# Kernel tuning notes

Hardware: AMD Instinct MI355X
Metric: run time of the kernel (lower is better)

Reference implementation:

```python
import jax, jax.numpy as jnp
import numpy as np

H = 256            # hidden_size
S = 4              # num_of_steps
B = 512            # reactions
N_MOLS = B * S     # 2048 molecules
ATOMS_PER_MOL = 32
N_ATOMS = N_MOLS * ATOMS_PER_MOL   # 65536
BONDS_PER_MOL = 64
N_BONDS = N_MOLS * BONDS_PER_MOL   # 131072 directed bonds (+1 pad row)
MAX_NB = 6
ATOM_FDIM = 133
BOND_FDIM = 147
DEPTH = 3
N_ITERS = 3  # Set2Set iterations


def setup_inputs() -> dict:
    key = jax.random.key(0)
    ks = jax.random.split(key, 20)
    def p(k, shape):
        return jax.random.normal(k, shape, jnp.float32) * 0.02
    inp = {}
    inp['f_atoms'] = jax.random.normal(ks[0], (N_ATOMS, ATOM_FDIM), jnp.float32)
    f_bonds = jax.random.normal(ks[1], (N_BONDS + 1, BOND_FDIM), jnp.float32)
    inp['f_bonds'] = f_bonds.at[0].set(0.0)  # chemprop zero pad row
    inp['a2b'] = jax.random.randint(ks[2], (N_ATOMS, MAX_NB), 0, N_BONDS + 1)
    inp['b2a'] = jax.random.randint(ks[3], (N_BONDS + 1,), 0, N_ATOMS)
    inp['b2revb'] = jax.random.randint(ks[4], (N_BONDS + 1,), 0, N_BONDS + 1)
    # MPN weights (bias=False for W_i/W_h as in args.bias default)
    inp['W_i'] = p(ks[5], (BOND_FDIM, H))
    inp['W_h'] = p(ks[6], (H, H))
    inp['W_o'] = p(ks[7], (ATOM_FDIM + H, H)); inp['b_o'] = jnp.zeros((H,), jnp.float32)
    # NNAttention over steps
    inp['W_nn0'] = p(ks[8], (2 * H, H));  inp['b_nn0'] = jnp.zeros((H,), jnp.float32)
    inp['W_nn0s'] = p(ks[9], (H, H));     inp['b_nn0s'] = jnp.zeros((H,), jnp.float32)
    inp['W_nn1'] = p(ks[10], (S * H, H)); inp['b_nn1'] = jnp.zeros((H,), jnp.float32)
    # node Set2Set (LSTM: input 2H -> hidden H) + condenser
    inp['lstm_n_Wih'] = p(ks[11], (4 * H, 2 * H))
    inp['lstm_n_Whh'] = p(ks[12], (4 * H, H))
    inp['lstm_n_b'] = jnp.zeros((4 * H,), jnp.float32)
    inp['node_cond_W'] = p(ks[13], (2 * H, H)); inp['node_cond_b'] = jnp.zeros((H,), jnp.float32)
    # graph (step) Set2Set + condenser
    inp['lstm_g_Wih'] = p(ks[14], (4 * H, 2 * H))
    inp['lstm_g_Whh'] = p(ks[15], (4 * H, H))
    inp['lstm_g_b'] = jnp.zeros((4 * H,), jnp.float32)
    inp['graph_cond_W'] = p(ks[16], (2 * H, H)); inp['graph_cond_b'] = jnp.zeros((H,), jnp.float32)
    return inp


def set2set(feat, Wih, Whh, b):
    # feat: [M, N, D]; LSTM n_layers=1, PyTorch gate order i,f,g,o
    M, N, D = feat.shape
    h = jnp.zeros((M, D), feat.dtype)
    c = jnp.zeros((M, D), feat.dtype)
    q_star = jnp.zeros((M, 2 * D), feat.dtype)
    for _ in range(N_ITERS):
        gates = q_star @ Wih.T + h @ Whh.T + b
        i, f, g, o = jnp.split(gates, 4, axis=-1)
        c = jax.nn.sigmoid(f) * c + jax.nn.sigmoid(i) * jnp.tanh(g)
        h = jax.nn.sigmoid(o) * jnp.tanh(c)
        q = h
        alpha = jax.nn.softmax(jnp.einsum('md,mnd->mn', q, feat), axis=1)
        readout = jnp.einsum('mn,mnd->md', alpha, feat)
        q_star = jnp.concatenate([q, readout], axis=-1)
    return q_star


def nn_attention(h, W0, b0, W0s, b0s, W1, b1):
    # vectorized form of the Attention module's s1/s2 double loop
    Bm, Sm, D = h.shape
    h1 = jnp.broadcast_to(h[:, :, None, :], (Bm, Sm, Sm, D))
    h2 = jnp.broadcast_to(h[:, None, :, :], (Bm, Sm, Sm, D))
    pair = jnp.concatenate([h1, h2], -1) @ W0 + b0          # [B,S,S,D] NN0(cat(h_s1,h_s2))
    self_o = h @ W0s + b0s                                   # [B,S,D]   NN0_self(h_s1)
    diag = jnp.eye(Sm, dtype=bool)[None, :, :, None]
    out = jnp.where(diag, self_o[:, :, None, :], pair)       # diagonal uses NN0_self
    return out.reshape(Bm, Sm, Sm * D) @ W1 + b1             # NN1 over s2-concat


def reference(f_atoms, f_bonds, a2b, b2a, b2revb, W_i, W_h, W_o, b_o,
              W_nn0, b_nn0, W_nn0s, b_nn0s, W_nn1, b_nn1,
              lstm_n_Wih, lstm_n_Whh, lstm_n_b, node_cond_W, node_cond_b,
              lstm_g_Wih, lstm_g_Whh, lstm_g_b, graph_cond_W, graph_cond_b):
    # --- bond message passing (chemprop, atom_messages=False) ---
    inp = f_bonds @ W_i                       # [NB+1, H], row 0 = 0 (no bias)
    message = jax.nn.relu(inp)
    message = message.at[0].set(0.0)          # keep pad row zero
    for _ in range(DEPTH - 1):
        a_message = message[a2b].sum(axis=1)          # gather+sum: [NA, H]
        msg = a_message[b2a] - message[b2revb]        # [NB+1, H]
        message = jax.nn.relu(inp + msg @ W_h)
        message = message.at[0].set(0.0)
    nei = message[a2b].sum(axis=1)                    # [NA, H]
    atom_h = jax.nn.relu(jnp.concatenate([f_atoms, nei], -1) @ W_o + b_o)
    # --- node readout: Set2Set per molecule + condenser ---
    feat = atom_h.reshape(N_MOLS, ATOMS_PER_MOL, H)
    mol = set2set(feat, lstm_n_Wih, lstm_n_Whh, lstm_n_b) @ node_cond_W + node_cond_b
    # --- step attention (NNAttention over num_of_steps) ---
    steps = mol.reshape(B, S, H)
    steps = nn_attention(steps, W_nn0, b_nn0, W_nn0s, b_nn0s, W_nn1, b_nn1)
    # --- step readout: Set2Set over steps + condenser ---
    out = set2set(steps, lstm_g_Wih, lstm_g_Whh, lstm_g_b) @ graph_cond_W + graph_cond_b
    return out  # [B, H]
```

## Files before the change

kernel.cpp:

```cpp
#include <hip/hip_runtime.h>
#include <math.h>

#define H 256
#define S_STEPS 4
#define B_RXN 512
#define N_MOLS 2048
#define ATOMS_PER_MOL 32
#define N_ATOMS 65536
#define N_BONDS 131072
#define NBP1 131073
#define MAX_NB 6
#define ATOM_FDIM 133
#define BOND_FDIM 147
#define DEPTH 3
#define N_ITERS 3

typedef unsigned short bf16u;
typedef __attribute__((ext_vector_type(8))) short short8v;
typedef __attribute__((ext_vector_type(4))) float f32x4;

__device__ __forceinline__ float b2f(bf16u u) {
    union { unsigned int i; float f; } c; c.i = ((unsigned int)u) << 16; return c.f;
}
__device__ __forceinline__ bf16u f2b(float f) {
    union { float f; unsigned int i; } c; c.f = f;
    unsigned int i = c.i;
    return (bf16u)((i + 0x7FFFu + ((i >> 16) & 1u)) >> 16);
}
__device__ __forceinline__ unsigned int relu2bf(unsigned int w) {
    unsigned int lo = w & 0xFFFFu, hi = w >> 16;
    if (lo & 0x8000u) lo = 0u;
    if (hi & 0x8000u) hi = 0u;
    return lo | (hi << 16);
}

template<int MODE, bool RELUA>
__global__ __launch_bounds__(512) void dense_gemm_k(
    const bf16u* __restrict__ A1,
    const bf16u* __restrict__ A2,
    const bf16u* __restrict__ WT,
    const float* __restrict__ bias,
    bf16u* __restrict__ outb,
    int M)
{
    constexpr int KP = (MODE == 0) ? 160 : ((MODE == 1) ? 256 : 416);
    constexpr int NS = KP / 32;
    __shared__ bf16u As[128][40];
    __shared__ bf16u Bs[256][40];

    const int tid = threadIdx.x;
    const int lane = tid & 63, w = tid >> 6;
    const int wr = w >> 2, wc = w & 3;
    const int m0 = blockIdx.x * 128;
    const int ar = tid >> 2, q8 = (tid & 3) * 8;
    const int br = tid >> 1, bh = (tid & 1) * 16;
    const int arow = m0 + ar;
    const bool rok = arow < M;
    const int lr = lane & 15, lk = (lane >> 4) * 8;
    const uint4 z4 = {0u, 0u, 0u, 0u};

    auto loadA = [&](int s) -> uint4 {
        const int kc = s * 32 + q8;
        if (MODE == 2) {
            return (kc < 160) ? *(const uint4*)(A1 + (size_t)arow * 160 + kc)
                              : *(const uint4*)(A2 + (size_t)arow * 256 + (kc - 160));
        } else {
            constexpr int LDA = (MODE == 0) ? 160 : 256;
            return rok ? *(const uint4*)(A1 + (size_t)arow * LDA + kc) : z4;
        }
    };
    auto loadB0 = [&](int s) { return *(const uint4*)(WT + (size_t)br * KP + s * 32 + bh); };
    auto loadB1 = [&](int s) { return *(const uint4*)(WT + (size_t)br * KP + s * 32 + bh + 8); };
    auto writeAB = [&](uint4 va, uint4 vb0, uint4 vb1) {
        if (RELUA) {
            va.x = relu2bf(va.x); va.y = relu2bf(va.y);
            va.z = relu2bf(va.z); va.w = relu2bf(va.w);
        }
        *(uint4*)&As[ar][q8] = va;
        *(uint4*)&Bs[br][bh] = vb0;
        *(uint4*)&Bs[br][bh + 8] = vb1;
    };

    f32x4 acc[4][4];
    const f32x4 zf = {0.f, 0.f, 0.f, 0.f};
    #pragma unroll
    for (int i = 0; i < 4; ++i)
        #pragma unroll
        for (int j = 0; j < 4; ++j) acc[i][j] = zf;

    writeAB(loadA(0), loadB0(0), loadB1(0));
    __syncthreads();

    for (int s = 0; s < NS; ++s) {
        const bool pf = (s + 1 < NS);
        uint4 va = z4, vb0 = z4, vb1 = z4;
        if (pf) { va = loadA(s + 1); vb0 = loadB0(s + 1); vb1 = loadB1(s + 1); }

        short8v a[4], b[4];
        #pragma unroll
        for (int mf = 0; mf < 4; ++mf)
            a[mf] = *(const short8v*)&As[wr * 64 + mf * 16 + lr][lk];
        #pragma unroll
        for (int nf = 0; nf < 4; ++nf)
            b[nf] = *(const short8v*)&Bs[wc * 64 + nf * 16 + lr][lk];
        #pragma unroll
        for (int mf = 0; mf < 4; ++mf)
            #pragma unroll
            for (int nf = 0; nf < 4; ++nf)
                acc[mf][nf] = __builtin_amdgcn_mfma_f32_16x16x32_bf16(
                    a[mf], b[nf], acc[mf][nf], 0, 0, 0);
        __syncthreads();
        if (pf) {
            writeAB(va, vb0, vb1);
            __syncthreads();
        }
    }

    const int rbase = (lane >> 4) * 4;
    #pragma unroll
    for (int mf = 0; mf < 4; ++mf) {
        #pragma unroll
        for (int nf = 0; nf < 4; ++nf) {
            const int col = wc * 64 + nf * 16 + lr;
            #pragma unroll
            for (int r = 0; r < 4; ++r) {
                const int row = m0 + wr * 64 + mf * 16 + rbase + r;
                if (row >= M) continue;
                float v = acc[mf][nf][r];
                const size_t off = (size_t)row * H + col;
                if (MODE == 2) {
                    v += bias[col];
                    outb[off] = f2b(fmaxf(v, 0.f));
                } else {
                    outb[off] = f2b(v);
                }
            }
        }
    }
}

__global__ __launch_bounds__(256) void combine_k(
    const bf16u* __restrict__ inp, const bf16u* __restrict__ AP,
    const bf16u* __restrict__ MW,
    const int* __restrict__ b2a, const int* __restrict__ b2revb,
    bf16u* __restrict__ msg)
{
    int idx = blockIdx.x * 256 + threadIdx.x;
    if (idx >= NBP1 * 32) return;
    int b = idx >> 5, c = (idx & 31) * 8;
    bf16u* op = msg + (size_t)b * H + c;
    if (b == 0) {
        *(uint4*)op = make_uint4(0u, 0u, 0u, 0u);
        return;
    }
    int a = b2a[b], rb = b2revb[b];
    uint4 ui = *(const uint4*)(inp + (size_t)b * H + c);
    uint4 up = *(const uint4*)(AP + (size_t)a * H + c);
    uint4 um = *(const uint4*)(MW + (size_t)rb * H + c);
    uint4 o;
    unsigned int* pi = &ui.x; unsigned int* pp = &up.x;
    unsigned int* pm = &um.x; unsigned int* po = &o.x;
    #pragma unroll
    for (int t = 0; t < 4; ++t) {
        float lo = b2f((bf16u)(pi[t] & 0xFFFFu)) + b2f((bf16u)(pp[t] & 0xFFFFu))
                 - b2f((bf16u)(pm[t] & 0xFFFFu));
        float hi = b2f((bf16u)(pi[t] >> 16)) + b2f((bf16u)(pp[t] >> 16))
                 - b2f((bf16u)(pm[t] >> 16));
        lo = fmaxf(lo, 0.f); hi = fmaxf(hi, 0.f);
        po[t] = (unsigned int)f2b(lo) | ((unsigned int)f2b(hi) << 16);
    }
    *(uint4*)op = o;
}

template<bool BIAS>
__global__ __launch_bounds__(256) void lin64_k(
    const float* __restrict__ A1, int lda1, int KA1,
    const float* __restrict__ A2, int lda2,
    const bf16u* __restrict__ WT, int ldw,
    const float* __restrict__ bias,
    float* __restrict__ C, int ldc, int K)
{
    __shared__ bf16u As[64][40];
    __shared__ bf16u Bs[64][40];
    const int tid = threadIdx.x;
    const int lane = tid & 63, w = tid >> 6;
    const int m0 = blockIdx.x * 64;
    const int col0 = blockIdx.y * 64;
    const int ar = tid >> 2, kq8 = (tid & 3) * 8;
    const int lr = lane & 15, lk = (lane >> 4) * 8;

    f32x4 acc[4];
    const f32x4 zf = {0.f, 0.f, 0.f, 0.f};
    #pragma unroll
    for (int j = 0; j < 4; ++j) acc[j] = zf;

    for (int k0 = 0; k0 < K; k0 += 32) {
        const float* src = (k0 < KA1)
            ? (A1 + (size_t)(m0 + ar) * lda1 + k0 + kq8)
            : (A2 + (size_t)(m0 + ar) * lda2 + (k0 - KA1) + kq8);
        float4 f0 = *(const float4*)src;
        float4 f1 = *(const float4*)(src + 4);
        ushort4 s0, s1;
        s0.x = f2b(f0.x); s0.y = f2b(f0.y); s0.z = f2b(f0.z); s0.w = f2b(f0.w);
        s1.x = f2b(f1.x); s1.y = f2b(f1.y); s1.z = f2b(f1.z); s1.w = f2b(f1.w);
        *(ushort4*)&As[ar][kq8] = s0;
        *(ushort4*)&As[ar][kq8 + 4] = s1;
        *(uint4*)&Bs[ar][kq8] = *(const uint4*)(WT + (size_t)(col0 + ar) * ldw + k0 + kq8);
        __syncthreads();

        short8v a = *(const short8v*)&As[w * 16 + lr][lk];
        short8v b[4];
        #pragma unroll
        for (int nf = 0; nf < 4; ++nf)
            b[nf] = *(const short8v*)&Bs[nf * 16 + lr][lk];
        #pragma unroll
        for (int nf = 0; nf < 4; ++nf)
            acc[nf] = __builtin_amdgcn_mfma_f32_16x16x32_bf16(a, b[nf], acc[nf], 0, 0, 0);
        __syncthreads();
    }

    const int rbase = (lane >> 4) * 4;
    #pragma unroll
    for (int nf = 0; nf < 4; ++nf) {
        const int col = col0 + nf * 16 + lr;
        #pragma unroll
        for (int r = 0; r < 4; ++r) {
            const int row = m0 + w * 16 + rbase + r;
            float v = acc[nf][r];
            if (BIAS) v += bias[col];
            C[(size_t)row * ldc + col] = v;
        }
    }
}

__device__ __forceinline__ float sigm(float x) { return 1.f / (1.f + expf(-x)); }

__global__ __launch_bounds__(256) void gates_lstm_k(
    const float* __restrict__ QSTAR,
    const float* __restrict__ Hc,
    const float* __restrict__ Cc,
    const bf16u* __restrict__ WT,
    const float* __restrict__ bias,
    float* __restrict__ Hn,
    float* __restrict__ Cn,
    int M)
{
    __shared__ bf16u As[64][40];
    __shared__ bf16u Bs[64][40];
    const int tid = threadIdx.x;
    const int lane = tid & 63, w = tid >> 6;
    const int m0 = blockIdx.x * 64;
    const int db = blockIdx.y;
    const int ar = tid >> 2, q8 = (tid & 3) * 8;
    const int lr = lane & 15, lk = (lane >> 4) * 8;

    f32x4 acc[4];
    const f32x4 zf = {0.f, 0.f, 0.f, 0.f};
    #pragma unroll
    for (int g = 0; g < 4; ++g) acc[g] = zf;

    for (int k0 = 0; k0 < 768; k0 += 32) {
        const float* src = (k0 < 512)
            ? QSTAR + (size_t)(m0 + ar) * 512 + k0 + q8
            : Hc + (size_t)(m0 + ar) * 256 + (k0 - 512) + q8;
        float4 f0 = *(const float4*)src;
        float4 f1 = *(const float4*)(src + 4);
        ushort4 s0, s1;
        s0.x = f2b(f0.x); s0.y = f2b(f0.y); s0.z = f2b(f0.z); s0.w = f2b(f0.w);
        s1.x = f2b(f1.x); s1.y = f2b(f1.y); s1.z = f2b(f1.z); s1.w = f2b(f1.w);
        *(ushort4*)&As[ar][q8] = s0;
        *(ushort4*)&As[ar][q8 + 4] = s1;
        {
            int rho = tid >> 2;
            int g = rho >> 4, cn = rho & 15;
            *(uint4*)&Bs[rho][q8] =
                *(const uint4*)(WT + (size_t)(g * 256 + db * 16 + cn) * 768 + k0 + q8);
        }
        __syncthreads();
        short8v a = *(const short8v*)&As[w * 16 + lr][lk];
        #pragma unroll
        for (int g = 0; g < 4; ++g) {
            short8v b = *(const short8v*)&Bs[g * 16 + lr][lk];
            acc[g] = __builtin_amdgcn_mfma_f32_16x16x32_bf16(a, b, acc[g], 0, 0, 0);
        }
        __syncthreads();
    }

    const int rbase = (lane >> 4) * 4;
    const int d = db * 16 + lr;
    const float bi = bias[d], bf = bias[256 + d], bg = bias[512 + d], bo = bias[768 + d];
    #pragma unroll
    for (int r = 0; r < 4; ++r) {
        const int row = m0 + w * 16 + rbase + r;
        float i_ = acc[0][r] + bi;
        float f_ = acc[1][r] + bf;
        float g_ = acc[2][r] + bg;
        float o_ = acc[3][r] + bo;
        float cv = sigm(f_) * Cc[(size_t)row * 256 + d] + sigm(i_) * tanhf(g_);
        Cn[(size_t)row * 256 + d] = cv;
        Hn[(size_t)row * 256 + d] = sigm(o_) * tanhf(cv);
    }
}

__global__ __launch_bounds__(256) void prep_wt_k(const float* __restrict__ W,
                                                 bf16u* __restrict__ WT, int K, int KP)
{
    int idx = blockIdx.x * 256 + threadIdx.x;
    if (idx >= 256 * KP) return;
    int n = idx / KP, k = idx - n * KP;
    WT[idx] = (k < K) ? f2b(W[(size_t)k * H + n]) : (bf16u)0;
}

__global__ __launch_bounds__(256) void prep_wto_k(const float* __restrict__ Wo,
                                                  bf16u* __restrict__ WT)
{
    int idx = blockIdx.x * 256 + threadIdx.x;
    if (idx >= 256 * 416) return;
    int n = idx / 416, k = idx - n * 416;
    float v = 0.f;
    if (k < ATOM_FDIM) v = Wo[(size_t)k * H + n];
    else if (k >= 160) v = Wo[(size_t)(ATOM_FDIM + k - 160) * H + n];
    WT[idx] = f2b(v);
}

#define SZ_WTG   786432
#define SZ_WTNC  131072
#define SZ_WTPQS 196608
#define SZ_WTN1  262144
#define SZ_WTGC  131072
__global__ __launch_bounds__(256) void prep_mid_k(
    const float* __restrict__ Wih_n, const float* __restrict__ Whh_n,
    const float* __restrict__ Wih_g, const float* __restrict__ Whh_g,
    const float* __restrict__ ncW,  const float* __restrict__ Wnn0,
    const float* __restrict__ Wnn0s, const float* __restrict__ Wnn1,
    const float* __restrict__ gcW,  const float* __restrict__ b_nn0s,
    bf16u* __restrict__ WTG_N, bf16u* __restrict__ WTG_G,
    bf16u* __restrict__ WT_NC, bf16u* __restrict__ WT_PQS,
    bf16u* __restrict__ WT_N1, bf16u* __restrict__ WT_GC,
    float* __restrict__ BIAS_PQS)
{
    int idx = blockIdx.x * 256 + threadIdx.x;
    if (idx < SZ_WTG) {
        int n = idx / 768, k = idx - n * 768;
        WTG_N[idx] = f2b(k < 512 ? Wih_n[(size_t)n * 512 + k] : Whh_n[(size_t)n * 256 + (k - 512)]);
        return;
    }
    idx -= SZ_WTG;
    if (idx < SZ_WTG) {
        int n = idx / 768, k = idx - n * 768;
        WTG_G[idx] = f2b(k < 512 ? Wih_g[(size_t)n * 512 + k] : Whh_g[(size_t)n * 256 + (k - 512)]);
        return;
    }
    idx -= SZ_WTG;
    if (idx < SZ_WTNC) {
        int n = idx / 512, k = idx - n * 512;
        WT_NC[idx] = f2b(ncW[(size_t)k * 256 + n]);
        return;
    }
    idx -= SZ_WTNC;
    if (idx < SZ_WTPQS) {
        int n = idx / 256, k = idx - n * 256;
        float v;
        if (n < 256)      v = Wnn0[(size_t)k * 256 + n];
        else if (n < 512) v = Wnn0[(size_t)(256 + k) * 256 + (n - 256)];
        else              v = Wnn0s[(size_t)k * 256 + (n - 512)];
        WT_PQS[idx] = f2b(v);
        return;
    }
    idx -= SZ_WTPQS;
    if (idx < SZ_WTN1) {
        int n = idx / 1024, k = idx - n * 1024;
        WT_N1[idx] = f2b(Wnn1[(size_t)k * 256 + n]);
        return;
    }
    idx -= SZ_WTN1;
    if (idx < SZ_WTGC) {
        int n = idx / 512, k = idx - n * 512;
        WT_GC[idx] = f2b(gcW[(size_t)k * 256 + n]);
        return;
    }
    idx -= SZ_WTGC;
    if (idx < 768) BIAS_PQS[idx] = (idx < 512) ? 0.f : b_nn0s[idx - 512];
}
#define PREP_MID_TOTAL (2 * SZ_WTG + SZ_WTNC + SZ_WTPQS + SZ_WTN1 + SZ_WTGC + 768)

__global__ __launch_bounds__(256) void prep_feat16_k(const float* __restrict__ F,
                                                     bf16u* __restrict__ O,
                                                     int rows, int K)
{
    int idx = blockIdx.x * 256 + threadIdx.x;
    if (idx >= rows * 160) return;
    int r = idx / 160, c = idx - r * 160;
    O[idx] = (c < K) ? f2b(F[(size_t)r * K + c]) : (bf16u)0;
}

__global__ __launch_bounds__(256) void gather6_bf16_k(const bf16u* __restrict__ msg,
                                                      const int* __restrict__ a2b,
                                                      bf16u* __restrict__ outb)
{
    int idx = blockIdx.x * 256 + threadIdx.x;
    if (idx >= N_ATOMS * (H / 8)) return;
    int na = idx >> 5, c = idx & 31;
    const int* nb = a2b + (size_t)na * MAX_NB;
    float s[8] = {0.f, 0.f, 0.f, 0.f, 0.f, 0.f, 0.f, 0.f};
    #pragma unroll
    for (int j = 0; j < MAX_NB; ++j) {
        uint4 u = *(const uint4*)(msg + (size_t)nb[j] * H + c * 8);
        s[0] += b2f((bf16u)(u.x & 0xFFFFu)); s[1] += b2f((bf16u)(u.x >> 16));
        s[2] += b2f((bf16u)(u.y & 0xFFFFu)); s[3] += b2f((bf16u)(u.y >> 16));
        s[4] += b2f((bf16u)(u.z & 0xFFFFu)); s[5] += b2f((bf16u)(u.z >> 16));
        s[6] += b2f((bf16u)(u.w & 0xFFFFu)); s[7] += b2f((bf16u)(u.w >> 16));
    }
    uint4 o;
    o.x = (unsigned int)f2b(s[0]) | ((unsigned int)f2b(s[1]) << 16);
    o.y = (unsigned int)f2b(s[2]) | ((unsigned int)f2b(s[3]) << 16);
    o.z = (unsigned int)f2b(s[4]) | ((unsigned int)f2b(s[5]) << 16);
    o.w = (unsigned int)f2b(s[6]) | ((unsigned int)f2b(s[7]) << 16);
    *(uint4*)(outb + (size_t)na * H + c * 8) = o;
}

__global__ __launch_bounds__(256) void zero_f32_k(float* __restrict__ p, int n)
{
    int idx = blockIdx.x * 256 + threadIdx.x;
    if (idx < n) p[idx] = 0.f;
}

template<bool BF16F>
__global__ __launch_bounds__(256) void s2s_attn_k(const void* __restrict__ featv,
                                                  const float* __restrict__ h,
                                                  float* __restrict__ q_star, int Nn)
{
    int m = blockIdx.x;
    int t = threadIdx.x;
    int lane = t & 63, wave = t >> 6;
    __shared__ float sc[32];
    const bf16u* fb = (const bf16u*)featv;
    const float* ff = (const float*)featv;
    const size_t fbase = (size_t)m * Nn * H;
    const float* hm = h + (size_t)m * H;
    for (int n = wave; n < Nn; n += 4) {
        float p = 0.f;
        if (BF16F) {
            ushort4 u = *(const ushort4*)(fb + fbase + (size_t)n * H + lane * 4);
            const float4 h4 = *(const float4*)(hm + lane * 4);
            p = b2f(u.x) * h4.x + b2f(u.y) * h4.y + b2f(u.z) * h4.z + b2f(u.w) * h4.w;
        } else {
            const float* fr = ff + fbase + (size_t)n * H;
            #pragma unroll
            for (int u = 0; u < 4; ++u) p += fr[lane * 4 + u] * hm[lane * 4 + u];
        }
        #pragma unroll
        for (int o = 32; o >= 1; o >>= 1) p += __shfl_xor(p, o);
        if (lane == 0) sc[n] = p;
    }
    __syncthreads();
    float mx = -1e30f;
    for (int n = 0; n < Nn; ++n) mx = fmaxf(mx, sc[n]);
    float ssum = 0.f, r = 0.f;
    for (int n = 0; n < Nn; ++n) {
        float a = expf(sc[n] - mx);
        ssum += a;
        float fv = BF16F ? b2f(fb[fbase + (size_t)n * H + t]) : ff[fbase + (size_t)n * H + t];
        r += a * fv;
    }
    r /= ssum;
    q_star[(size_t)m * (2 * H) + t] = hm[t];
    q_star[(size_t)m * (2 * H) + H + t] = r;
}

__global__ __launch_bounds__(256) void build_x_k(const float* __restrict__ PQS,
                                                 const float* __restrict__ b0,
                                                 float* __restrict__ X)
{
    int idx = blockIdx.x * 256 + threadIdx.x;
    if (idx >= B_RXN * S_STEPS * S_STEPS * H) return;
    int d  = idx & 255;
    int s2 = (idx >> 8) & 3;
    int s1 = (idx >> 10) & 3;
    int b  = idx >> 12;
    float v;
    if (s1 == s2) v = PQS[((size_t)(b * S_STEPS + s1)) * 768 + 512 + d];
    else v = PQS[((size_t)(b * S_STEPS + s1)) * 768 + d]
           + PQS[((size_t)(b * S_STEPS + s2)) * 768 + 256 + d] + b0[d];
    X[idx] = v;
}

extern "C" void kernel_launch(void* const* d_in, const int* in_sizes, int n_in,
                              void* d_out, int out_size, void* d_ws, size_t ws_size,
                              hipStream_t stream)
{
    const float* f_atoms   = (const float*)d_in[0];
    const float* f_bonds   = (const float*)d_in[1];
    const int*   a2b       = (const int*)d_in[2];
    const int*   b2a       = (const int*)d_in[3];
    const int*   b2revb    = (const int*)d_in[4];
    const float* W_i       = (const float*)d_in[5];
    const float* W_h       = (const float*)d_in[6];
    const float* W_o       = (const float*)d_in[7];
    const float* b_o       = (const float*)d_in[8];
    const float* W_nn0     = (const float*)d_in[9];
    const float* b_nn0     = (const float*)d_in[10];
    const float* W_nn0s    = (const float*)d_in[11];
    const float* b_nn0s    = (const float*)d_in[12];
    const float* W_nn1     = (const float*)d_in[13];
    const float* b_nn1     = (const float*)d_in[14];
    const float* lstm_n_Wih = (const float*)d_in[15];
    const float* lstm_n_Whh = (const float*)d_in[16];
    const float* lstm_n_b   = (const float*)d_in[17];
    const float* node_cond_W = (const float*)d_in[18];
    const float* node_cond_b = (const float*)d_in[19];
    const float* lstm_g_Wih = (const float*)d_in[20];
    const float* lstm_g_Whh = (const float*)d_in[21];
    const float* lstm_g_b   = (const float*)d_in[22];
    const float* graph_cond_W = (const float*)d_in[23];
    const float* graph_cond_b = (const float*)d_in[24];
    float* out = (float*)d_out;

    const size_t SZB = (size_t)NBP1 * H * sizeof(bf16u);
    char* base = (char*)d_ws;
    bf16u* INP  = (bf16u*)(base);
    bf16u* MSG  = (bf16u*)(base + SZB);
    bf16u* MW   = (bf16u*)(base + 2 * SZB);
    bf16u* AMSG = (bf16u*)(base + 3 * SZB);
    bf16u* WT_I = (bf16u*)(base + 3 * SZB + 33554432);
    bf16u* WT_H = (bf16u*)(base + 3 * SZB + 33636352);
    bf16u* WT_O = (bf16u*)(base + 3 * SZB + 33767424);
    bf16u* FB16 = MW;
    bf16u* FA16 = MW;
    bf16u* ATOMH16 = (bf16u*)(base);
    float* SMALL = (float*)(base + SZB);
    float* HN     = SMALL + 2097152;
    float* CN     = SMALL + 2621440;
    float* QSTARN = SMALL + 3145728;
    float* MOL    = SMALL + 4194304;
    float* PQS    = SMALL + 4718592;
    float* XBUF   = SMALL + 6291456;
    float* STEPS  = SMALL + 8388608;
    float* HG     = SMALL + 8912896;
    float* CG     = SMALL + 9043968;
    float* QSTARG = SMALL + 9175040;
    float* HN2    = SMALL + 10485760;
    float* CN2    = SMALL + 11010048;
    float* HG2    = SMALL + 11534336;
    float* CG2    = SMALL + 11665408;
    char* sm2 = base + 2 * SZB + 25165824;
    bf16u* WTG_N   = (bf16u*)(sm2);
    bf16u* WTG_G   = (bf16u*)(sm2 + 1572864);
    bf16u* WT_NC   = (bf16u*)(sm2 + 3145728);
    bf16u* WT_PQS  = (bf16u*)(sm2 + 3407872);
    bf16u* WT_N1   = (bf16u*)(sm2 + 3801088);
    bf16u* WT_GC   = (bf16u*)(sm2 + 4325376);
    float* BIAS_PQS = (float*)(sm2 + 4587520);

    dim3 blk(256), blk5(512);
    const int MB_BOND = (NBP1 + 127) / 128;
    const int MB_ATOM = N_ATOMS / 128;
    const int G_GATH = (N_ATOMS * (H / 8) + 255) / 256;
    const int G_COMB = (NBP1 * 32 + 255) / 256;

    prep_wt_k<<<(256 * 160 + 255) / 256, blk, 0, stream>>>(W_i, WT_I, BOND_FDIM, 160);
    prep_wt_k<<<(256 * 256 + 255) / 256, blk, 0, stream>>>(W_h, WT_H, H, 256);
    prep_wto_k<<<(256 * 416 + 255) / 256, blk, 0, stream>>>(W_o, WT_O);
    prep_feat16_k<<<(int)(((size_t)NBP1 * 160 + 255) / 256), blk, 0, stream>>>(
        f_bonds, FB16, NBP1, BOND_FDIM);

    dense_gemm_k<0, false><<<MB_BOND, blk5, 0, stream>>>(
        FB16, nullptr, WT_I, nullptr, INP, NBP1);

    dense_gemm_k<1, true><<<MB_BOND, blk5, 0, stream>>>(
        INP, nullptr, WT_H, nullptr, MW, NBP1);
    gather6_bf16_k<<<G_GATH, blk, 0, stream>>>(MW, a2b, AMSG);
    combine_k<<<G_COMB, blk, 0, stream>>>(INP, AMSG, MW, b2a, b2revb, MSG);
    dense_gemm_k<1, false><<<MB_BOND, blk5, 0, stream>>>(
        MSG, nullptr, WT_H, nullptr, MW, NBP1);
    gather6_bf16_k<<<G_GATH, blk, 0, stream>>>(MW, a2b, AMSG);
    combine_k<<<G_COMB, blk, 0, stream>>>(INP, AMSG, MW, b2a, b2revb, MSG);

    gather6_bf16_k<<<G_GATH, blk, 0, stream>>>(MSG, a2b, AMSG);

    prep_feat16_k<<<(N_ATOMS * 160 + 255) / 256, blk, 0, stream>>>(
        f_atoms, FA16, N_ATOMS, ATOM_FDIM);
    prep_mid_k<<<(PREP_MID_TOTAL + 255) / 256, blk, 0, stream>>>(
        lstm_n_Wih, lstm_n_Whh, lstm_g_Wih, lstm_g_Whh,
        node_cond_W, W_nn0, W_nn0s, W_nn1, graph_cond_W, b_nn0s,
        WTG_N, WTG_G, WT_NC, WT_PQS, WT_N1, WT_GC, BIAS_PQS);

    dense_gemm_k<2, false><<<MB_ATOM, blk5, 0, stream>>>(
        FA16, AMSG, WT_O, b_o, ATOMH16, N_ATOMS);

    zero_f32_k<<<(2097152 + 255) / 256, blk, 0, stream>>>(HN, 2097152);
    {
        float *hc = HN, *cc = CN, *hn = HN2, *cn = CN2;
        for (int it = 0; it < N_ITERS; ++it) {
            gates_lstm_k<<<dim3(N_MOLS / 64, 16), blk, 0, stream>>>(
                QSTARN, hc, cc, WTG_N, lstm_n_b, hn, cn, N_MOLS);
            s2s_attn_k<true><<<N_MOLS, blk, 0, stream>>>(ATOMH16, hn, QSTARN, ATOMS_PER_MOL);
            float* t;
            t = hc; hc = hn; hn = t;
            t = cc; cc = cn; cn = t;
        }
    }
    lin64_k<true><<<dim3(N_MOLS / 64, 4), blk, 0, stream>>>(
        QSTARN, 2 * H, 2 * H, QSTARN, 2 * H, WT_NC, 2 * H, node_cond_b, MOL, H, 2 * H);

    lin64_k<true><<<dim3(N_MOLS / 64, 12), blk, 0, stream>>>(
        MOL, H, H, MOL, H, WT_PQS, H, BIAS_PQS, PQS, 3 * H, H);
    build_x_k<<<(B_RXN * 16 * H) / 256, blk, 0, stream>>>(PQS, b_nn0, XBUF);
    lin64_k<true><<<dim3(N_MOLS / 64, 4), blk, 0, stream>>>(
        XBUF, S_STEPS * H, S_STEPS * H, XBUF, S_STEPS * H, WT_N1, S_STEPS * H, b_nn1,
        STEPS, H, S_STEPS * H);

    zero_f32_k<<<(524288 + 255) / 256, blk, 0, stream>>>(HG, 524288);
    {
        float *hc = HG, *cc = CG, *hn = HG2, *cn = CG2;
        for (int it = 0; it < N_ITERS; ++it) {
            gates_lstm_k<<<dim3(B_RXN / 64, 16), blk, 0, stream>>>(
                QSTARG, hc, cc, WTG_G, lstm_g_b, hn, cn, B_RXN);
            s2s_attn_k<false><<<B_RXN, blk, 0, stream>>>(STEPS, hn, QSTARG, S_STEPS);
            float* t;
            t = hc; hc = hn; hn = t;
            t = cc; cc = cn; cn = t;
        }
    }

    lin64_k<true><<<dim3(B_RXN / 64, 4), blk, 0, stream>>>(
        QSTARG, 2 * H, 2 * H, QSTARG, 2 * H, WT_GC, 2 * H, graph_cond_b, out, H, 2 * H);
}
```

Baseline: 676.9 us.

## Skip first Set2Set LSTM GEMM via closed-form zero-state step; simplify GEMM loop

Because the Set2Set LSTM starts from zero h, c and q_star, the first iteration's gate GEMM reduces to the bias. A small broadcast kernel now computes h0 and c0 from the bias directly, replacing the zero-fill kernel and the first gates_lstm launch in both node and graph readouts. Separately, the dense GEMM drops its register prefetch double-buffering in favour of a simple load-sync-compute-sync loop. That lowers register pressure but no longer overlaps global loads with MFMA work.

```diff
diff --git a/kernel.cpp b/kernel.cpp
--- a/kernel.cpp
+++ b/kernel.cpp
@@ -44,7 +44,6 @@
     int M)
 {
     constexpr int KP = (MODE == 0) ? 160 : ((MODE == 1) ? 256 : 416);
-    constexpr int NS = KP / 32;
     __shared__ bf16u As[128][40];
     __shared__ bf16u Bs[256][40];
 
@@ -59,42 +58,36 @@
     const int lr = lane & 15, lk = (lane >> 4) * 8;
     const uint4 z4 = {0u, 0u, 0u, 0u};
 
-    auto loadA = [&](int s) -> uint4 {
-        const int kc = s * 32 + q8;
+    f32x4 acc[4][4];
+    const f32x4 zf = {0.f, 0.f, 0.f, 0.f};
+    #pragma unroll
+    for (int i = 0; i < 4; ++i)
+        #pragma unroll
+        for (int j = 0; j < 4; ++j) acc[i][j] = zf;
+
+    for (int k0 = 0; k0 < KP; k0 += 32) {
+        const int kc = k0 + q8;
+        uint4 va;
         if (MODE == 2) {
-            return (kc < 160) ? *(const uint4*)(A1 + (size_t)arow * 160 + kc)
-                              : *(const uint4*)(A2 + (size_t)arow * 256 + (kc - 160));
+            va = (kc < 160) ? *(const uint4*)(A1 + (size_t)arow * 160 + kc)
+                            : *(const uint4*)(A2 + (size_t)arow * 256 + (kc - 160));
         } else {
             constexpr int LDA = (MODE == 0) ? 160 : 256;
-            return rok ? *(const uint4*)(A1 + (size_t)arow * LDA + kc) : z4;
-        }
-    };
-    auto loadB0 = [&](int s) { return *(const uint4*)(WT + (size_t)br * KP + s * 32 + bh); };
-    auto loadB1 = [&](int s) { return *(const uint4*)(WT + (size_t)br * KP + s * 32 + bh + 8); };
-    auto writeAB = [&](uint4 va, uint4 vb0, uint4 vb1) {
+            va = rok ? *(const uint4*)(A1 + (size_t)arow * LDA + kc) : z4;
+        }
         if (RELUA) {
             va.x = relu2bf(va.x); va.y = relu2bf(va.y);
             va.z = relu2bf(va.z); va.w = relu2bf(va.w);
         }
         *(uint4*)&As[ar][q8] = va;
-        *(uint4*)&Bs[br][bh] = vb0;
-        *(uint4*)&Bs[br][bh + 8] = vb1;
-    };
-
-    f32x4 acc[4][4];
-    const f32x4 zf = {0.f, 0.f, 0.f, 0.f};
-    #pragma unroll
-    for (int i = 0; i < 4; ++i)
-        #pragma unroll
-        for (int j = 0; j < 4; ++j) acc[i][j] = zf;
-
-    writeAB(loadA(0), loadB0(0), loadB1(0));
-    __syncthreads();
-
-    for (int s = 0; s < NS; ++s) {
-        const bool pf = (s + 1 < NS);
-        uint4 va = z4, vb0 = z4, vb1 = z4;
-        if (pf) { va = loadA(s + 1); vb0 = loadB0(s + 1); vb1 = loadB1(s + 1); }
+        {
+            const bf16u* bp = WT + (size_t)br * KP + k0 + bh;
+            uint4 b0 = *(const uint4*)(bp);
+            uint4 b1 = *(const uint4*)(bp + 8);
+            *(uint4*)&Bs[br][bh] = b0;
+            *(uint4*)&Bs[br][bh + 8] = b1;
+        }
+        __syncthreads();
 
         short8v a[4], b[4];
         #pragma unroll
@@ -110,10 +103,6 @@
                 acc[mf][nf] = __builtin_amdgcn_mfma_f32_16x16x32_bf16(
                     a[mf], b[nf], acc[mf][nf], 0, 0, 0);
         __syncthreads();
-        if (pf) {
-            writeAB(va, vb0, vb1);
-            __syncthreads();
-        }
     }
 
     const int rbase = (lane >> 4) * 4;
@@ -302,6 +291,19 @@
     }
 }
 
+__global__ __launch_bounds__(256) void lstm0_bcast_k(const float* __restrict__ bias,
+                                                     float* __restrict__ Hn,
+                                                     float* __restrict__ Cn, int M)
+{
+    int idx = blockIdx.x * 256 + threadIdx.x;
+    if (idx >= M * 256) return;
+    int d = idx & 255;
+    float c0 = sigm(bias[d]) * tanhf(bias[512 + d]);
+    float h0 = sigm(bias[768 + d]) * tanhf(c0);
+    Cn[idx] = c0;
+    Hn[idx] = h0;
+}
+
 __global__ __launch_bounds__(256) void prep_wt_k(const float* __restrict__ W,
                                                  bf16u* __restrict__ WT, int K, int KP)
 {
@@ -417,12 +419,6 @@
     o.z = (unsigned int)f2b(s[4]) | ((unsigned int)f2b(s[5]) << 16);
     o.w = (unsigned int)f2b(s[6]) | ((unsigned int)f2b(s[7]) << 16);
     *(uint4*)(outb + (size_t)na * H + c * 8) = o;
-}
-
-__global__ __launch_bounds__(256) void zero_f32_k(float* __restrict__ p, int n)
-{
-    int idx = blockIdx.x * 256 + threadIdx.x;
-    if (idx < n) p[idx] = 0.f;
 }
 
 template<bool BF16F>
@@ -588,10 +584,11 @@
     dense_gemm_k<2, false><<<MB_ATOM, blk5, 0, stream>>>(
         FA16, AMSG, WT_O, b_o, ATOMH16, N_ATOMS);
 
-    zero_f32_k<<<(2097152 + 255) / 256, blk, 0, stream>>>(HN, 2097152);
     {
+        lstm0_bcast_k<<<(N_MOLS * H + 255) / 256, blk, 0, stream>>>(lstm_n_b, HN, CN, N_MOLS);
+        s2s_attn_k<true><<<N_MOLS, blk, 0, stream>>>(ATOMH16, HN, QSTARN, ATOMS_PER_MOL);
         float *hc = HN, *cc = CN, *hn = HN2, *cn = CN2;
-        for (int it = 0; it < N_ITERS; ++it) {
+        for (int it = 1; it < N_ITERS; ++it) {
             gates_lstm_k<<<dim3(N_MOLS / 64, 16), blk, 0, stream>>>(
                 QSTARN, hc, cc, WTG_N, lstm_n_b, hn, cn, N_MOLS);
             s2s_attn_k<true><<<N_MOLS, blk, 0, stream>>>(ATOMH16, hn, QSTARN, ATOMS_PER_MOL);
@@ -610,10 +607,11 @@
         XBUF, S_STEPS * H, S_STEPS * H, XBUF, S_STEPS * H, WT_N1, S_STEPS * H, b_nn1,
         STEPS, H, S_STEPS * H);
 
-    zero_f32_k<<<(524288 + 255) / 256, blk, 0, stream>>>(HG, 524288);
     {
+        lstm0_bcast_k<<<(B_RXN * H + 255) / 256, blk, 0, stream>>>(lstm_g_b, HG, CG, B_RXN);
+        s2s_attn_k<false><<<B_RXN, blk, 0, stream>>>(STEPS, HG, QSTARG, S_STEPS);
         float *hc = HG, *cc = CG, *hn = HG2, *cn = CG2;
-        for (int it = 0; it < N_ITERS; ++it) {
+        for (int it = 1; it < N_ITERS; ++it) {
             gates_lstm_k<<<dim3(B_RXN / 64, 16), blk, 0, stream>>>(
                 QSTARG, hc, cc, WTG_G, lstm_g_b, hn, cn, B_RXN);
             s2s_attn_k<false><<<B_RXN, blk, 0, stream>>>(STEPS, hn, QSTARG, S_STEPS);
```

Result: faster. 611.7 us (-9.6%).
